# Kernel tuning notes

Measured on AMD Instinct MI355X. Metric: run time of the kernel, lower is better.

## Reference

```python
import jax, jax.numpy as jnp
import numpy as np

B, T, E, H = 8, 2048, 1024, 128

def setup_inputs() -> dict:
    key = jax.random.key(0)
    kx, kq, kk, kv = jax.random.split(key, 4)
    x = jax.random.normal(kx, (B, T, E), dtype=jnp.float32)
    # Linear(E, H, bias=False) weights, stored as (E, H) so y = x @ W
    s = 1.0 / np.sqrt(E)
    Wq = jax.random.normal(kq, (E, H), dtype=jnp.float32) * s
    Wk = jax.random.normal(kk, (E, H), dtype=jnp.float32) * s
    Wv = jax.random.normal(kv, (E, H), dtype=jnp.float32) * s
    return {"x": x, "Wq": Wq, "Wk": Wk, "Wv": Wv}

def reference(x, Wq, Wk, Wv):
    # x: (B, T, E)
    Tcur = x.shape[1]
    q = jnp.einsum('bte,eh->bth', x, Wq)
    k = jnp.einsum('bte,eh->bth', x, Wk)
    v = jnp.einsum('bte,eh->bth', x, Wv)
    scores = jnp.einsum('bqh,bkh->bqk', q, k)  # (B, T, T)
    # NOTE: source multiplies by x.shape[2]**0.5 where x.shape[2] == T here
    scores = scores * jnp.sqrt(jnp.asarray(Tcur, dtype=scores.dtype))
    causal = jnp.tril(jnp.ones((Tcur, Tcur), dtype=bool))
    scores = jnp.where(causal, scores, -jnp.inf)
    attn = jax.nn.softmax(scores, axis=2)
    # dropout p=0.0 -> identity
    return jnp.einsum('bqk,bkh->bqh', attn, v)
```

## Files before the change

kernel.cpp:

```cpp
#include <hip/hip_runtime.h>
#include <hip/hip_bf16.h>
#include <math.h>

#define B_ 8
#define T_ 2048
#define E_ 1024
#define H_ 128
#define M_ (B_*T_)
#define SCALE_ 45.25483399593904f
#define SEG_ 4

typedef __attribute__((ext_vector_type(8))) short bf16x8;
typedef __attribute__((ext_vector_type(4))) float f32x4;

#define mfma16(A, Bv, C) __builtin_amdgcn_mfma_f32_16x16x32_bf16((A), (Bv), (C), 0, 0, 0)

#define FRAGW(g, kc, lane)  ((((size_t)(g)*32 + (kc))*64 + (lane))*8)
#define FRAGK(b, kt16, kc, lane) (((((size_t)(b)*128 + (kt16))*4 + (kc))*64 + (lane))*8)
#define FRAGV(b, ht, kt32, lane) (((((size_t)(b)*8 + (ht))*64 + (kt32))*64 + (lane))*8)

__device__ __forceinline__ ushort bf16_rne(float f) {
  unsigned u = __float_as_uint(f);
  u += 0x7fffu + ((u >> 16) & 1u);
  return (ushort)(u >> 16);
}
__device__ __forceinline__ float bf16_tof(ushort h) {
  return __uint_as_float(((unsigned)h) << 16);
}

__device__ __forceinline__ void lds_barrier() {
  asm volatile("s_waitcnt lgkmcnt(0)" ::: "memory");
  __builtin_amdgcn_s_barrier();
}

__global__ __launch_bounds__(256) void wsplit(
    const float* __restrict__ Wq, const float* __restrict__ Wk,
    const float* __restrict__ Wv,
    ushort* __restrict__ whT, ushort* __restrict__ wlT)
{
  const int idx  = blockIdx.x * 256 + threadIdx.x;
  const int mat  = idx >> 14;
  const int rem  = idx & 16383;
  const int nt   = rem >> 11;
  const int kc   = (rem >> 6) & 31;
  const int lane = rem & 63;
  const int quad = lane >> 4, l15 = lane & 15;
  const float* W = (mat == 0) ? Wq : (mat == 1) ? Wk : Wv;
  const int n  = nt * 16 + l15;
  const int k0 = kc * 32 + quad * 8;
  bf16x8 hv, lv;
  #pragma unroll
  for (int j = 0; j < 8; ++j) {
    const float f = W[(size_t)(k0 + j) * H_ + n];
    const ushort h = bf16_rne(f);
    hv[j] = (short)h;
    lv[j] = (short)bf16_rne(f - bf16_tof(h));
  }
  *(bf16x8*)(whT + (size_t)idx * 8) = hv;
  *(bf16x8*)(wlT + (size_t)idx * 8) = lv;
}

#define CVT8W(F0, F1, DSTOFF) do {                                            \
    const float f_[8] = {(F0).x, (F0).y, (F0).z, (F0).w,                      \
                         (F1).x, (F1).y, (F1).z, (F1).w};                     \
    bf16x8 hv_, lv_;                                                          \
    _Pragma("unroll")                                                         \
    for (int jj_ = 0; jj_ < 8; ++jj_) {                                       \
      const ushort h_ = bf16_rne(f_[jj_]);                                    \
      hv_[jj_] = (short)h_;                                                   \
      lv_[jj_] = (short)bf16_rne(f_[jj_] - bf16_tof(h_));                     \
    }                                                                         \
    *(bf16x8*)&SM[(DSTOFF) + ca * 8] = hv_;                                   \
    *(bf16x8*)&SM[(DSTOFF) + 2048 + ca * 8] = lv_;                            \
  } while (0)

#define APH(CUR, P, MT) (*(const bf16x8*)&SM[(CUR)*16384 + (P)*4096 + \
    (((MT)*4 + quad)*16 + (l15 ^ quad))*8])
#define ALH(CUR, P, MT) (*(const bf16x8*)&SM[(CUR)*16384 + (P)*4096 + 2048 + \
    (((MT)*4 + quad)*16 + (l15 ^ quad))*8])

#define MPHASE(CUR, P, BH0, BH1, BH2, BL0, BL1) do {                          \
    bf16x8 ah_[4], al_[4];                                                    \
    _Pragma("unroll")                                                         \
    for (int mt_ = 0; mt_ < 4; ++mt_) {                                       \
      ah_[mt_] = APH(CUR, P, mt_);                                            \
      al_[mt_] = ALH(CUR, P, mt_);                                            \
    }                                                                         \
    __builtin_amdgcn_s_setprio(1);                                            \
    _Pragma("unroll")                                                         \
    for (int mt_ = 0; mt_ < 4; ++mt_) {                                       \
      acc[0][mt_] = mfma16(ah_[mt_], BH0, acc[0][mt_]);                       \
      acc[0][mt_] = mfma16(ah_[mt_], BL0, acc[0][mt_]);                       \
      acc[0][mt_] = mfma16(al_[mt_], BH0, acc[0][mt_]);                       \
      acc[1][mt_] = mfma16(ah_[mt_], BH1, acc[1][mt_]);                       \
      acc[1][mt_] = mfma16(ah_[mt_], BL1, acc[1][mt_]);                       \
      acc[1][mt_] = mfma16(al_[mt_], BH1, acc[1][mt_]);                       \
      acc[2][mt_] = mfma16(ah_[mt_], BH2, acc[2][mt_]);                       \
    }                                                                         \
    __builtin_amdgcn_s_setprio(0);                                            \
  } while (0)

#define BLOADX(KCN0) do {                                                     \
    _Pragma("unroll")                                                         \
    for (int kch_ = 0; kch_ < 2; ++kch_) {                                    \
      const int kcn_ = (KCN0) + kch_;                                         \
      bhX[kch_*3+0] = *(const bf16x8*)(whT + FRAGW(gq,     kcn_, lane));      \
      bhX[kch_*3+1] = *(const bf16x8*)(whT + FRAGW(gq + 4, kcn_, lane));      \
      bhX[kch_*3+2] = *(const bf16x8*)(whT + FRAGW(gv,     kcn_, lane));      \
      blX[kch_*2+0] = *(const bf16x8*)(wlT + FRAGW(gq,     kcn_, lane));      \
      blX[kch_*2+1] = *(const bf16x8*)(wlT + FRAGW(gq + 4, kcn_, lane));      \
    }                                                                         \
  } while (0)

#define BLOADY(KCN0) do {                                                     \
    _Pragma("unroll")                                                         \
    for (int kch_ = 0; kch_ < 2; ++kch_) {                                    \
      const int kcn_ = (KCN0) + kch_;                                         \
      bhY[kch_*3+0] = *(const bf16x8*)(whT + FRAGW(gq,     kcn_, lane));      \
      bhY[kch_*3+1] = *(const bf16x8*)(whT + FRAGW(gq + 4, kcn_, lane));      \
      bhY[kch_*3+2] = *(const bf16x8*)(whT + FRAGW(gv,     kcn_, lane));      \
      blY[kch_*2+0] = *(const bf16x8*)(wlT + FRAGW(gq,     kcn_, lane));      \
      blY[kch_*2+1] = *(const bf16x8*)(wlT + FRAGW(gq + 4, kcn_, lane));      \
    }                                                                         \
  } while (0)

#define XLOAD(SOFF) do {                                                      \
    xf0 = *(const float4*)(xrow + (SOFF));                                    \
    xf1 = *(const float4*)(xrow + (SOFF) + 4);                                \
    xf2 = *(const float4*)(xrow + (SOFF) + 32);                               \
    xf3 = *(const float4*)(xrow + (SOFF) + 36);                               \
    xf4 = *(const float4*)(xrow + (SOFF) + 64);                               \
    xf5 = *(const float4*)(xrow + (SOFF) + 68);                               \
    xf6 = *(const float4*)(xrow + (SOFF) + 96);                               \
    xf7 = *(const float4*)(xrow + (SOFF) + 100);                              \
  } while (0)

#define PSTEP8(S, CUR, NXT) do {                                              \
    MPHASE(CUR, 0, bhX[0], bhX[1], bhX[2], blX[0], blX[1]);                   \
    MPHASE(CUR, 1, bhX[3], bhX[4], bhX[5], blX[2], blX[3]);                   \
    if ((S) + 1 < 8) {                                                        \
      BLOADX(4*((S)+1));                                                      \
      CVT8W(xf0, xf1, (NXT)*16384);                                           \
      CVT8W(xf2, xf3, (NXT)*16384 + 4096);                                    \
    }                                                                         \
    MPHASE(CUR, 2, bhY[0], bhY[1], bhY[2], blY[0], blY[1]);                   \
    MPHASE(CUR, 3, bhY[3], bhY[4], bhY[5], blY[2], blY[3]);                   \
    if ((S) + 1 < 8) {                                                        \
      BLOADY(4*((S)+1) + 2);                                                  \
      CVT8W(xf4, xf5, (NXT)*16384 + 8192);                                    \
      CVT8W(xf6, xf7, (NXT)*16384 + 12288);                                   \
    }                                                                         \
    if ((S) + 2 < 8) XLOAD(128*((S)+2));                                      \
    lds_barrier();                                                            \
  } while (0)

__global__ __launch_bounds__(256, 2) void proj_fused(
    const float* __restrict__ x,
    const ushort* __restrict__ whT, const ushort* __restrict__ wlT,
    ushort* __restrict__ qh, ushort* __restrict__ ql,
    ushort* __restrict__ kfh, ushort* __restrict__ kfl,
    ushort* __restrict__ vF)
{
  const int m0   = blockIdx.x * 64;
  const int half = blockIdx.y;
  const int tid  = threadIdx.x;
  const int wave = tid >> 6, lane = tid & 63;
  const int quad = lane >> 4, l15 = lane & 15;

  __shared__ __align__(16) ushort SM[32768];

  f32x4 acc[3][4];
  #pragma unroll
  for (int j = 0; j < 3; ++j)
    #pragma unroll
    for (int mt = 0; mt < 4; ++mt) acc[j][mt] = (f32x4){0.f, 0.f, 0.f, 0.f};

  const int arow  = tid >> 2;
  const int akoff = (tid & 3) * 8;
  const int ca    = ((arow >> 4) * 4 + (tid & 3)) * 16
                    + ((arow & 15) ^ (tid & 3));
  const int gq    = half * 8 + wave;
  const int gv    = 16 + half * 4 + wave;

  const float* xrow = x + (size_t)(m0 + arow) * E_ + akoff;

  float4 xf0, xf1, xf2, xf3, xf4, xf5, xf6, xf7;
  bf16x8 bhX[6], blX[4], bhY[6], blY[4];

  {
    const float4 a0 = *(const float4*)(xrow);
    const float4 a1 = *(const float4*)(xrow + 4);
    const float4 a2 = *(const float4*)(xrow + 32);
    const float4 a3 = *(const float4*)(xrow + 36);
    const float4 a4 = *(const float4*)(xrow + 64);
    const float4 a5 = *(const float4*)(xrow + 68);
    const float4 a6 = *(const float4*)(xrow + 96);
    const float4 a7 = *(const float4*)(xrow + 100);
    CVT8W(a0, a1, 0);
    CVT8W(a2, a3, 4096);
    CVT8W(a4, a5, 8192);
    CVT8W(a6, a7, 12288);
    XLOAD(128);
    BLOADX(0);
    BLOADY(2);
  }
  lds_barrier();

  int s = 0;
  while (true) {
    PSTEP8(s, 0, 1); if (++s == 8) break;
    PSTEP8(s, 1, 0); if (++s == 8) break;
  }

  {
    ushort* TB = SM;
    const int colbase = wave * 16 + l15;
    const int bb = m0 >> 11, t0 = m0 & 2047;
    #pragma unroll
    for (int pass = 0; pass < 2; ++pass) {
      __syncthreads();
      #pragma unroll
      for (int j = 0; j < 2; ++j)
        #pragma unroll
        for (int mt = 0; mt < 4; ++mt)
          #pragma unroll
          for (int r = 0; r < 4; ++r) {
            const float a = acc[j][mt][r];
            const ushort h = bf16_rne(a);
            const ushort val = pass ? bf16_rne(a - bf16_tof(h)) : h;
            TB[(mt * 16 + quad * 4 + r) * 136 + colbase + j * 64] = val;
          }
      __syncthreads();
      if (half == 0) {
        const int row = tid >> 2, c0 = (tid & 3) * 32;
        ushort* dst = (pass ? ql : qh) + (size_t)(m0 + row) * H_ + c0;
        #pragma unroll
        for (int u = 0; u < 4; ++u)
          *(bf16x8*)(dst + u * 8) = *(const bf16x8*)&TB[row * 136 + c0 + u * 8];
      } else {
        ushort* dstb = (pass ? kfl : kfh) + FRAGK(bb, t0 >> 4, 0, 0) + tid * 32;
        const int kt16l = tid >> 6;
        const int kcc   = (tid >> 4) & 3;
        const int lane0 = (tid & 15) * 4;
        #pragma unroll
        for (int u = 0; u < 4; ++u) {
          const int l  = lane0 + u;
          const int key = kt16l * 16 + (l & 15);
          const int h0  = kcc * 32 + (l >> 4) * 8;
          *(bf16x8*)(dstb + u * 8) = *(const bf16x8*)&TB[key * 136 + h0];
        }
      }
    }
  }
  __syncthreads();
  {
    ushort* smT = SM;
    const int lh = wave * 16 + l15;
    #pragma unroll
    for (int mt = 0; mt < 4; ++mt)
      #pragma unroll
      for (int r = 0; r < 4; ++r)
        smT[lh * 72 + mt * 16 + quad * 4 + r] = bf16_rne(acc[2][mt][r]);
    __syncthreads();
    const int bb = m0 >> 11, t0 = m0 & 2047;
    #pragma unroll
    for (int u = 0; u < 2; ++u) {
      const int c    = u * 256 + tid;
      const int lht  = c >> 7;
      const int ktl  = (c >> 6) & 1;
      const int lv   = c & 63;
      const int qv   = lv >> 4, l15v = lv & 15;
      *(bf16x8*)(vF + FRAGV(bb, half * 4 + lht, (t0 >> 5) + ktl, lv)) =
          *(const bf16x8*)&smT[(lht * 16 + l15v) * 72 + ktl * 32 + qv * 8];
    }
  }
}

__global__ __launch_bounds__(256) void attn_flash(
    const ushort* __restrict__ qh, const ushort* __restrict__ ql,
    const ushort* __restrict__ kfh, const ushort* __restrict__ kfl,
    const ushort* __restrict__ vF,
    ushort* __restrict__ Opart, float* __restrict__ mlpart)
{
  const int b    = (int)blockIdx.x & 7;
  const int seg  = (int)blockIdx.x >> 3;
  const int qt   = 31 - (int)blockIdx.y;
  const int q0   = qt * 64;
  const int tid  = threadIdx.x;
  const int wave = tid >> 6, lane = tid & 63;
  const int quad = lane >> 4, l15 = lane & 15;
  const f32x4 z4 = (f32x4){0.f, 0.f, 0.f, 0.f};

  __shared__ __align__(16) unsigned smPw[1280];
  __shared__ __align__(16) ushort  smO[8704];
  unsigned* pw = smPw + wave * 320;

  const int ntiles = 2 * qt + 2;
  const int cnt    = (ntiles + SEG_ - 1) >> 2;
  const int jt0    = seg * cnt;
  const int jt1    = (jt0 + cnt < ntiles) ? (jt0 + cnt) : ntiles;

  const int q0w = q0 + wave * 16;
  const int ntw = ((q0w + 15) >> 5) + 1;
  const size_t pidx = ((size_t)(b * 128 + qt * 4 + wave)) * SEG_ + seg;
  ushort* op = Opart + pidx * 2048;
  float*  ml = mlpart + pidx * 32;

  if (jt0 >= jt1) {
    const bf16x8 zz = {0, 0, 0, 0, 0, 0, 0, 0};
    #pragma unroll
    for (int u = 0; u < 4; ++u)
      *(bf16x8*)(op + lane * 32 + u * 8) = zz;
    if (lane < 32) ml[lane] = (lane & 1) ? 0.f : -1e30f;
    return;
  }

  const size_t base = (size_t)b * T_ * H_;

  const ushort* qhp = qh + base + (size_t)(q0w + l15) * H_ + quad * 8;
  const ushort* qlp = ql + base + (size_t)(q0w + l15) * H_ + quad * 8;
  bf16x8 Qh[4], Ql[4];
  #pragma unroll
  for (int c = 0; c < 4; ++c) {
    Qh[c] = *(const bf16x8*)(qhp + c * 32);
    Ql[c] = *(const bf16x8*)(qlp + c * 32);
  }

  f32x4 O[8];
  #pragma unroll
  for (int i = 0; i < 8; ++i) O[i] = z4;
  float mst = -1e30f;
  float lst = 0.f;

  const size_t kvb = (size_t)b * 262144;
  const int jtc = (jt1 < ntw) ? jt1 : ntw;

  for (int jt = jt0; jt < jtc; ++jt) {
    const ushort* pKh = kfh + kvb + (size_t)jt * 4096;
    const ushort* pKl = kfl + kvb + (size_t)jt * 4096;
    const ushort* pV  = vF  + kvb + (size_t)jt * 512;
    const int k0 = jt * 32;

    f32x4 shh0 = z4, shh1 = z4, sx0 = z4, sx1 = z4;
    #pragma unroll
    for (int c = 0; c < 4; ++c) {
      const bf16x8 kh0 = *(const bf16x8*)(pKh + c * 512 + lane * 8);
      const bf16x8 kh1 = *(const bf16x8*)(pKh + (4 + c) * 512 + lane * 8);
      const bf16x8 kl0 = *(const bf16x8*)(pKl + c * 512 + lane * 8);
      const bf16x8 kl1 = *(const bf16x8*)(pKl + (4 + c) * 512 + lane * 8);
      shh0 = mfma16(kh0, Qh[c], shh0);
      shh1 = mfma16(kh1, Qh[c], shh1);
      sx0  = mfma16(kl0, Qh[c], sx0);
      sx1  = mfma16(kl1, Qh[c], sx1);
      sx0  = mfma16(kh0, Ql[c], sx0);
      sx1  = mfma16(kh1, Ql[c], sx1);
    }

    float r0[4], r1[4];
    #pragma unroll
    for (int r = 0; r < 4; ++r) {
      r0[r] = shh0[r] + sx0[r];
      r1[r] = shh1[r] + sx1[r];
    }
    if (jt == ntw - 1) {
      const int base0 = q0w + l15 - k0 - quad * 4;
      #pragma unroll
      for (int r = 0; r < 4; ++r) {
        if (r > base0)      r0[r] = -1e30f;
        if (r > base0 - 16) r1[r] = -1e30f;
      }
    }

    float pm = fmaxf(fmaxf(fmaxf(r0[0], r0[1]), fmaxf(r0[2], r0[3])),
                     fmaxf(fmaxf(r1[0], r1[1]), fmaxf(r1[2], r1[3])));
    pm = fmaxf(pm, __shfl_xor(pm, 16));
    pm = fmaxf(pm, __shfl_xor(pm, 32));

    const float mnew  = fmaxf(mst, pm);
    const float alpha = __expf((mst - mnew) * SCALE_);
    mst = mnew;

    float p0[4], p1[4];
    #pragma unroll
    for (int r = 0; r < 4; ++r) {
      p0[r] = __expf((r0[r] - mnew) * SCALE_);
      p1[r] = __expf((r1[r] - mnew) * SCALE_);
    }
    float sm = ((p0[0] + p0[1]) + (p0[2] + p0[3])) +
               ((p1[0] + p1[1]) + (p1[2] + p1[3]));
    sm += __shfl_xor(sm, 16);
    sm += __shfl_xor(sm, 32);
    lst = lst * alpha + sm;

    const unsigned w0 = (unsigned)bf16_rne(p0[0]) | ((unsigned)bf16_rne(p0[1]) << 16);
    const unsigned w1 = (unsigned)bf16_rne(p0[2]) | ((unsigned)bf16_rne(p0[3]) << 16);
    const unsigned w2 = (unsigned)bf16_rne(p1[0]) | ((unsigned)bf16_rne(p1[1]) << 16);
    const unsigned w3 = (unsigned)bf16_rne(p1[2]) | ((unsigned)bf16_rne(p1[3]) << 16);
    *(unsigned long long*)&pw[l15 * 20 + 2 * quad] =
        (unsigned long long)w0 | ((unsigned long long)w1 << 32);
    *(unsigned long long*)&pw[l15 * 20 + 8 + 2 * quad] =
        (unsigned long long)w2 | ((unsigned long long)w3 << 32);

    #pragma unroll
    for (int ct = 0; ct < 8; ++ct) {
      O[ct][0] *= alpha; O[ct][1] *= alpha;
      O[ct][2] *= alpha; O[ct][3] *= alpha;
    }
    const bf16x8 pB = *(const bf16x8*)&pw[l15 * 20 + 4 * quad];
    #pragma unroll
    for (int ct = 0; ct < 8; ++ct) {
      const bf16x8 vf = *(const bf16x8*)(pV + ct * 32768 + lane * 8);
      O[ct] = mfma16(vf, pB, O[ct]);
    }
  }

  {
    ushort* so = smO + wave * 2176;
    #pragma unroll
    for (int ct = 0; ct < 8; ++ct)
      #pragma unroll
      for (int r = 0; r < 4; ++r)
        so[l15 * 136 + ct * 16 + quad * 4 + r] = bf16_rne(O[ct][r]);
    #pragma unroll
    for (int u = 0; u < 4; ++u) {
      const int q_ = u * 4 + quad;
      *(bf16x8*)(op + q_ * 128 + l15 * 8) =
          *(const bf16x8*)&so[q_ * 136 + l15 * 8];
    }
  }
  if (quad == 0) {
    ml[l15 * 2]     = mst * SCALE_;
    ml[l15 * 2 + 1] = lst;
  }
}

__global__ __launch_bounds__(256) void attn_combine(
    const ushort* __restrict__ Opart, const float* __restrict__ mlpart,
    float* __restrict__ out)
{
  const int idx = blockIdx.x * 256 + threadIdx.x;
  const int c4  = idx & 31;
  const int r   = idx >> 5;
  const int t   = r & 2047;
  const int qt  = t >> 4, r16 = t & 15;
  const size_t pb = ((size_t)((r >> 11) * 128 + qt)) * SEG_;

  float m[SEG_], l[SEG_];
  #pragma unroll
  for (int s = 0; s < SEG_; ++s) {
    m[s] = mlpart[(pb + s) * 32 + r16 * 2];
    l[s] = mlpart[(pb + s) * 32 + r16 * 2 + 1];
  }
  float M = m[0];
  #pragma unroll
  for (int s = 1; s < SEG_; ++s) M = fmaxf(M, m[s]);
  float w[SEG_], L = 0.f;
  #pragma unroll
  for (int s = 0; s < SEG_; ++s) {
    w[s] = __expf(m[s] - M);
    L += l[s] * w[s];
  }
  float4 acc = make_float4(0.f, 0.f, 0.f, 0.f);
  #pragma unroll
  for (int s = 0; s < SEG_; ++s) {
    if (w[s] != 0.f) {
      const ushort4 o = *(const ushort4*)(Opart + (pb + s) * 2048 + r16 * 128 + c4 * 4);
      acc.x += w[s] * bf16_tof(o.x);
      acc.y += w[s] * bf16_tof(o.y);
      acc.z += w[s] * bf16_tof(o.z);
      acc.w += w[s] * bf16_tof(o.w);
    }
  }
  const float inv = 1.0f / L;
  *(float4*)(out + (size_t)r * H_ + c4 * 4) =
      make_float4(acc.x * inv, acc.y * inv, acc.z * inv, acc.w * inv);
}

extern "C" void kernel_launch(void* const* d_in, const int* in_sizes, int n_in,
                              void* d_out, int out_size, void* d_ws, size_t ws_size,
                              hipStream_t stream) {
  (void)in_sizes; (void)n_in; (void)out_size; (void)ws_size;
  const float* x  = (const float*)d_in[0];
  const float* Wq = (const float*)d_in[1];
  const float* Wk = (const float*)d_in[2];
  const float* Wv = (const float*)d_in[3];
  float* out = (float*)d_out;

  ushort* qhb = (ushort*)d_ws;
  ushort* qlb = qhb + (size_t)M_ * H_;
  ushort* kfh = qlb + (size_t)M_ * H_;
  ushort* kfl = kfh + (size_t)M_ * H_;
  ushort* vFb = kfl + (size_t)M_ * H_;
  ushort* whT = vFb + (size_t)M_ * H_;
  ushort* wlT = whT + (size_t)3 * H_ * E_;
  ushort* Opart = wlT + (size_t)3 * H_ * E_;
  float*  mlpart = (float*)(Opart + (size_t)B_ * 128 * SEG_ * 2048);

  wsplit<<<dim3(192), 256, 0, stream>>>(Wq, Wk, Wv, whT, wlT);
  proj_fused<<<dim3(M_/64, 2), 256, 0, stream>>>(x, whT, wlT,
                                                 qhb, qlb, kfh, kfl, vFb);
  attn_flash<<<dim3(B_*SEG_, 32), 256, 0, stream>>>(qhb, qlb, kfh, kfl, vFb,
                                                    Opart, mlpart);
  attn_combine<<<dim3(2048), 256, 0, stream>>>(Opart, mlpart, out);
}
```

Before: 165.1 us.

## Merge projection halves into one 512-thread block sharing the converted x tile

The projection kernel used to launch two 256-thread blocks per 64-row tile, one per output half, and each block loaded and bf16-split the same x rows on its own. Now a single 512-thread block has 8 waves, and each half of the waves handles one output half, so the x tile is loaded and converted once and shared through LDS. This halves the x reads from global memory and the split-conversion work per tile. The cost is larger blocks with more register pressure under launch_bounds(512,2), and the epilogue now writes Q and K into separate LDS regions.

```diff
diff --git a/kernel.cpp b/kernel.cpp
--- a/kernel.cpp
+++ b/kernel.cpp
@@ -60,7 +60,7 @@
   *(bf16x8*)(wlT + (size_t)idx * 8) = lv;
 }
 
-#define CVT8W(F0, F1, DSTOFF) do {                                            \
+#define CVT8W2(F0, F1, DSTOFF) do {                                           \
     const float f_[8] = {(F0).x, (F0).y, (F0).z, (F0).w,                      \
                          (F1).x, (F1).y, (F1).z, (F1).w};                     \
     bf16x8 hv_, lv_;                                                          \
@@ -70,8 +70,8 @@
       hv_[jj_] = (short)h_;                                                   \
       lv_[jj_] = (short)bf16_rne(f_[jj_] - bf16_tof(h_));                     \
     }                                                                         \
-    *(bf16x8*)&SM[(DSTOFF) + ca * 8] = hv_;                                   \
-    *(bf16x8*)&SM[(DSTOFF) + 2048 + ca * 8] = lv_;                            \
+    *(bf16x8*)&SM[(DSTOFF) + ca0 * 8] = hv_;                                  \
+    *(bf16x8*)&SM[(DSTOFF) + 2048 + ca0 * 8] = lv_;                           \
   } while (0)
 
 #define APH(CUR, P, MT) (*(const bf16x8*)&SM[(CUR)*16384 + (P)*4096 + \
@@ -124,15 +124,11 @@
     }                                                                         \
   } while (0)
 
-#define XLOAD(SOFF) do {                                                      \
-    xf0 = *(const float4*)(xrow + (SOFF));                                    \
-    xf1 = *(const float4*)(xrow + (SOFF) + 4);                                \
-    xf2 = *(const float4*)(xrow + (SOFF) + 32);                               \
-    xf3 = *(const float4*)(xrow + (SOFF) + 36);                               \
-    xf4 = *(const float4*)(xrow + (SOFF) + 64);                               \
-    xf5 = *(const float4*)(xrow + (SOFF) + 68);                               \
-    xf6 = *(const float4*)(xrow + (SOFF) + 96);                               \
-    xf7 = *(const float4*)(xrow + (SOFF) + 100);                              \
+#define XLOAD2(SOFF) do {                                                     \
+    xq0 = *(const float4*)(xrow2 + (SOFF));                                   \
+    xq1 = *(const float4*)(xrow2 + (SOFF) + 4);                               \
+    xq2 = *(const float4*)(xrow2 + (SOFF) + 64);                              \
+    xq3 = *(const float4*)(xrow2 + (SOFF) + 68);                              \
   } while (0)
 
 #define PSTEP8(S, CUR, NXT) do {                                              \
@@ -140,21 +136,17 @@
     MPHASE(CUR, 1, bhX[3], bhX[4], bhX[5], blX[2], blX[3]);                   \
     if ((S) + 1 < 8) {                                                        \
       BLOADX(4*((S)+1));                                                      \
-      CVT8W(xf0, xf1, (NXT)*16384);                                           \
-      CVT8W(xf2, xf3, (NXT)*16384 + 4096);                                    \
+      CVT8W2(xq0, xq1, (NXT)*16384 + p0*4096);                                \
+      CVT8W2(xq2, xq3, (NXT)*16384 + (p0 + 2)*4096);                          \
     }                                                                         \
     MPHASE(CUR, 2, bhY[0], bhY[1], bhY[2], blY[0], blY[1]);                   \
     MPHASE(CUR, 3, bhY[3], bhY[4], bhY[5], blY[2], blY[3]);                   \
-    if ((S) + 1 < 8) {                                                        \
-      BLOADY(4*((S)+1) + 2);                                                  \
-      CVT8W(xf4, xf5, (NXT)*16384 + 8192);                                    \
-      CVT8W(xf6, xf7, (NXT)*16384 + 12288);                                   \
-    }                                                                         \
-    if ((S) + 2 < 8) XLOAD(128*((S)+2));                                      \
+    if ((S) + 1 < 8) BLOADY(4*((S)+1) + 2);                                   \
+    if ((S) + 2 < 8) XLOAD2(128*((S)+2));                                     \
     lds_barrier();                                                            \
   } while (0)
 
-__global__ __launch_bounds__(256, 2) void proj_fused(
+__global__ __launch_bounds__(512, 2) void proj_fused(
     const float* __restrict__ x,
     const ushort* __restrict__ whT, const ushort* __restrict__ wlT,
     ushort* __restrict__ qh, ushort* __restrict__ ql,
@@ -162,10 +154,10 @@
     ushort* __restrict__ vF)
 {
   const int m0   = blockIdx.x * 64;
-  const int half = blockIdx.y;
   const int tid  = threadIdx.x;
   const int wave = tid >> 6, lane = tid & 63;
   const int quad = lane >> 4, l15 = lane & 15;
+  const int half = wave >> 2, w4 = wave & 3;
 
   __shared__ __align__(16) ushort SM[32768];
 
@@ -175,32 +167,27 @@
     #pragma unroll
     for (int mt = 0; mt < 4; ++mt) acc[j][mt] = (f32x4){0.f, 0.f, 0.f, 0.f};
 
-  const int arow  = tid >> 2;
-  const int akoff = (tid & 3) * 8;
-  const int ca    = ((arow >> 4) * 4 + (tid & 3)) * 16
-                    + ((arow & 15) ^ (tid & 3));
-  const int gq    = half * 8 + wave;
-  const int gv    = 16 + half * 4 + wave;
-
-  const float* xrow = x + (size_t)(m0 + arow) * E_ + akoff;
-
-  float4 xf0, xf1, xf2, xf3, xf4, xf5, xf6, xf7;
+  const int p0    = tid >> 8;
+  const int ca0   = tid & 255;
+  const int topc  = ca0 >> 4;
+  const int hi    = topc >> 2, koff = topc & 3;
+  const int arow  = hi * 16 + ((ca0 & 15) ^ koff);
+  const int gq    = half * 8 + w4;
+  const int gv    = 16 + half * 4 + w4;
+
+  const float* xrow2 = x + (size_t)(m0 + arow) * E_ + p0 * 32 + koff * 8;
+
+  float4 xq0, xq1, xq2, xq3;
   bf16x8 bhX[6], blX[4], bhY[6], blY[4];
 
   {
-    const float4 a0 = *(const float4*)(xrow);
-    const float4 a1 = *(const float4*)(xrow + 4);
-    const float4 a2 = *(const float4*)(xrow + 32);
-    const float4 a3 = *(const float4*)(xrow + 36);
-    const float4 a4 = *(const float4*)(xrow + 64);
-    const float4 a5 = *(const float4*)(xrow + 68);
-    const float4 a6 = *(const float4*)(xrow + 96);
-    const float4 a7 = *(const float4*)(xrow + 100);
-    CVT8W(a0, a1, 0);
-    CVT8W(a2, a3, 4096);
-    CVT8W(a4, a5, 8192);
-    CVT8W(a6, a7, 12288);
-    XLOAD(128);
+    const float4 a0 = *(const float4*)(xrow2);
+    const float4 a1 = *(const float4*)(xrow2 + 4);
+    const float4 a2 = *(const float4*)(xrow2 + 64);
+    const float4 a3 = *(const float4*)(xrow2 + 68);
+    CVT8W2(a0, a1, p0 * 4096);
+    CVT8W2(a2, a3, (p0 + 2) * 4096);
+    XLOAD2(128);
     BLOADX(0);
     BLOADY(2);
   }
@@ -213,8 +200,10 @@
   }
 
   {
-    ushort* TB = SM;
-    const int colbase = wave * 16 + l15;
+    ushort* TBq = SM;
+    ushort* TBk = SM + 8704;
+    ushort* TBw = half ? TBk : TBq;
+    const int colbase = w4 * 16 + l15;
     const int bb = m0 >> 11, t0 = m0 & 2047;
     #pragma unroll
     for (int pass = 0; pass < 2; ++pass) {
@@ -228,26 +217,27 @@
             const float a = acc[j][mt][r];
             const ushort h = bf16_rne(a);
             const ushort val = pass ? bf16_rne(a - bf16_tof(h)) : h;
-            TB[(mt * 16 + quad * 4 + r) * 136 + colbase + j * 64] = val;
+            TBw[(mt * 16 + quad * 4 + r) * 136 + colbase + j * 64] = val;
           }
       __syncthreads();
-      if (half == 0) {
+      if (tid < 256) {
         const int row = tid >> 2, c0 = (tid & 3) * 32;
         ushort* dst = (pass ? ql : qh) + (size_t)(m0 + row) * H_ + c0;
         #pragma unroll
         for (int u = 0; u < 4; ++u)
-          *(bf16x8*)(dst + u * 8) = *(const bf16x8*)&TB[row * 136 + c0 + u * 8];
+          *(bf16x8*)(dst + u * 8) = *(const bf16x8*)&TBq[row * 136 + c0 + u * 8];
       } else {
-        ushort* dstb = (pass ? kfl : kfh) + FRAGK(bb, t0 >> 4, 0, 0) + tid * 32;
-        const int kt16l = tid >> 6;
-        const int kcc   = (tid >> 4) & 3;
-        const int lane0 = (tid & 15) * 4;
+        const int tk = tid - 256;
+        ushort* dstb = (pass ? kfl : kfh) + FRAGK(bb, t0 >> 4, 0, 0) + tk * 32;
+        const int kt16l = tk >> 6;
+        const int kcc   = (tk >> 4) & 3;
+        const int lane0 = (tk & 15) * 4;
         #pragma unroll
         for (int u = 0; u < 4; ++u) {
           const int l  = lane0 + u;
           const int key = kt16l * 16 + (l & 15);
           const int h0  = kcc * 32 + (l >> 4) * 8;
-          *(bf16x8*)(dstb + u * 8) = *(const bf16x8*)&TB[key * 136 + h0];
+          *(bf16x8*)(dstb + u * 8) = *(const bf16x8*)&TBk[key * 136 + h0];
         }
       }
     }
@@ -265,13 +255,13 @@
     const int bb = m0 >> 11, t0 = m0 & 2047;
     #pragma unroll
     for (int u = 0; u < 2; ++u) {
-      const int c    = u * 256 + tid;
-      const int lht  = c >> 7;
+      const int c    = u * 512 + tid;
+      const int ht   = c >> 7;
       const int ktl  = (c >> 6) & 1;
       const int lv   = c & 63;
       const int qv   = lv >> 4, l15v = lv & 15;
-      *(bf16x8*)(vF + FRAGV(bb, half * 4 + lht, (t0 >> 5) + ktl, lv)) =
-          *(const bf16x8*)&smT[(lht * 16 + l15v) * 72 + ktl * 32 + qv * 8];
+      *(bf16x8*)(vF + FRAGV(bb, ht, (t0 >> 5) + ktl, lv)) =
+          *(const bf16x8*)&smT[(ht * 16 + l15v) * 72 + ktl * 32 + qv * 8];
     }
   }
 }
@@ -380,22 +370,22 @@
     const float alpha = __expf((mst - mnew) * SCALE_);
     mst = mnew;
 
-    float p0[4], p1[4];
+    float p0a[4], p1a[4];
     #pragma unroll
     for (int r = 0; r < 4; ++r) {
-      p0[r] = __expf((r0[r] - mnew) * SCALE_);
-      p1[r] = __expf((r1[r] - mnew) * SCALE_);
-    }
-    float sm = ((p0[0] + p0[1]) + (p0[2] + p0[3])) +
-               ((p1[0] + p1[1]) + (p1[2] + p1[3]));
+      p0a[r] = __expf((r0[r] - mnew) * SCALE_);
+      p1a[r] = __expf((r1[r] - mnew) * SCALE_);
+    }
+    float sm = ((p0a[0] + p0a[1]) + (p0a[2] + p0a[3])) +
+               ((p1a[0] + p1a[1]) + (p1a[2] + p1a[3]));
     sm += __shfl_xor(sm, 16);
     sm += __shfl_xor(sm, 32);
     lst = lst * alpha + sm;
 
-    const unsigned w0 = (unsigned)bf16_rne(p0[0]) | ((unsigned)bf16_rne(p0[1]) << 16);
-    const unsigned w1 = (unsigned)bf16_rne(p0[2]) | ((unsigned)bf16_rne(p0[3]) << 16);
-    const unsigned w2 = (unsigned)bf16_rne(p1[0]) | ((unsigned)bf16_rne(p1[1]) << 16);
-    const unsigned w3 = (unsigned)bf16_rne(p1[2]) | ((unsigned)bf16_rne(p1[3]) << 16);
+    const unsigned w0 = (unsigned)bf16_rne(p0a[0]) | ((unsigned)bf16_rne(p0a[1]) << 16);
+    const unsigned w1 = (unsigned)bf16_rne(p0a[2]) | ((unsigned)bf16_rne(p0a[3]) << 16);
+    const unsigned w2 = (unsigned)bf16_rne(p1a[0]) | ((unsigned)bf16_rne(p1a[1]) << 16);
+    const unsigned w3 = (unsigned)bf16_rne(p1a[2]) | ((unsigned)bf16_rne(p1a[3]) << 16);
     *(unsigned long long*)&pw[l15 * 20 + 2 * quad] =
         (unsigned long long)w0 | ((unsigned long long)w1 << 32);
     *(unsigned long long*)&pw[l15 * 20 + 8 + 2 * quad] =
@@ -497,8 +487,8 @@
   float*  mlpart = (float*)(Opart + (size_t)B_ * 128 * SEG_ * 2048);
 
   wsplit<<<dim3(192), 256, 0, stream>>>(Wq, Wk, Wv, whT, wlT);
-  proj_fused<<<dim3(M_/64, 2), 256, 0, stream>>>(x, whT, wlT,
-                                                 qhb, qlb, kfh, kfl, vFb);
+  proj_fused<<<dim3(M_/64), 512, 0, stream>>>(x, whT, wlT,
+                                              qhb, qlb, kfh, kfl, vFb);
   attn_flash<<<dim3(B_*SEG_, 32), 256, 0, stream>>>(qhb, qlb, kfh, kfl, vFb,
                                                     Opart, mlpart);
   attn_combine<<<dim3(2048), 256, 0, stream>>>(Opart, mlpart, out);
```

Result: no change. 165.0 us (-0.1%).
